# Kernel tuning notes

Measured on AMD Instinct MI355X. Metric: run time of the kernel, lower is better.

Reference implementation:

```python
import jax, jax.numpy as jnp
import numpy as np

B, S, H, FMAX, MAXSENT, NHEADS, FFN, SEP = 32, 2048, 768, 32, 64, 12, 3072, 102


def setup_inputs() -> dict:
    key = jax.random.key(0)
    ks = jax.random.split(key, 16)
    sc = 0.02
    ids = jax.random.randint(ks[0], (B, S), 1000, 30000)
    pos = jnp.arange(S)
    # SEP token every 32 positions -> 63 variable-span 'sentences' per row
    ids = jnp.where((pos[None, :] % 32 == 0) & (pos[None, :] > 0), SEP, ids)
    n = lambda k, shp: sc * jax.random.normal(k, shp, jnp.float32)
    return {
        "hidden1": jax.random.normal(ks[1], (B, S, H), jnp.float32),
        "fact_cls": jax.random.normal(ks[2], (B, FMAX, H), jnp.float32),
        "Wp": n(ks[3], (H, H)), "bp": jnp.zeros((H,), jnp.float32), "vp": n(ks[4], (H, 1)),
        "Wq": n(ks[5], (H, H)), "bq": jnp.zeros((H,), jnp.float32),
        "Wk": n(ks[6], (H, H)), "bk": jnp.zeros((H,), jnp.float32),
        "Wv": n(ks[7], (H, H)), "bv": jnp.zeros((H,), jnp.float32),
        "Wo": n(ks[8], (H, H)), "bo": jnp.zeros((H,), jnp.float32),
        "ln1g": jnp.ones((H,), jnp.float32), "ln1b": jnp.zeros((H,), jnp.float32),
        "Wf1": n(ks[9], (H, FFN)), "bf1": jnp.zeros((FFN,), jnp.float32),
        "Wf2": n(ks[10], (FFN, H)), "bf2": jnp.zeros((H,), jnp.float32),
        "ln2g": jnp.ones((H,), jnp.float32), "ln2b": jnp.zeros((H,), jnp.float32),
        "input_ids": ids,
        "facts_count": jax.random.randint(ks[11], (B,), 0, FMAX),
        "max_sent": MAXSENT,
        "sep_id": SEP,
    }


def _ln(x, g, b):
    mu = jnp.mean(x, axis=-1, keepdims=True)
    var = jnp.mean((x - mu) ** 2, axis=-1, keepdims=True)
    return (x - mu) * jax.lax.rsqrt(var + 1e-12) * g + b


def _forward(hidden1, fact_cls, Wp, bp, vp, Wq, bq, Wk, bk, Wv, bv, Wo, bo,
             ln1g, ln1b, Wf1, bf1, Wf2, bf2, ln2g, ln2b,
             input_ids, facts_count, max_sent, sep_id):
    B_, S_ = input_ids.shape
    H_ = hidden1.shape[-1]
    # ---- ragged sentence spans: tokens strictly between SEPs, starting at pos 1 ----
    is_sep = input_ids == sep_id                      # [B,S]
    n_sent = jnp.sum(is_sep, axis=-1)                 # [B]
    seg = jnp.cumsum(is_sep, axis=1) - is_sep         # exclusive cumsum: sentence id per token
    pos = jnp.arange(S_)
    valid = (pos[None, :] >= 1) & (~is_sep) & (seg < n_sent[:, None])
    nseg = B_ * max_sent
    seg_id = jnp.where(valid, jnp.arange(B_)[:, None] * max_sent + seg, nseg).reshape(-1)
    # ---- attention pooling per sentence (segment softmax) ----
    scores = jnp.squeeze(jnp.tanh(hidden1 @ Wp + bp) @ vp, -1).reshape(-1)  # [B*S]
    vflat = valid.reshape(-1)
    m = jax.ops.segment_max(scores, seg_id, num_segments=nseg + 1)
    e = jnp.where(vflat, jnp.exp(scores - m[seg_id]), 0.0)
    z = jax.ops.segment_sum(e, seg_id, num_segments=nseg + 1)
    z = jnp.where(z > 0, z, 1.0)
    w = e / z[seg_id]
    sent = jax.ops.segment_sum(w[:, None] * hidden1.reshape(-1, H_), seg_id,
                               num_segments=nseg + 1)[:nseg].reshape(B_, max_sent, H_)
    # zero-sentence rows fall back to CLS embedding in slot 0
    sent = sent.at[:, 0].set(jnp.where((n_sent == 0)[:, None], hidden1[:, 0], sent[:, 0]))
    n_eff = jnp.maximum(n_sent, 1)
    # ---- pack sentences then facts into dense zero-padded buffer ----
    FMAX_ = fact_cls.shape[1]
    L = max_sent + FMAX_
    bidx = jnp.arange(B_)[:, None]
    buf = jnp.zeros((B_, L + 1, H_), hidden1.dtype)  # extra trash column L
    spos = jnp.where(jnp.arange(max_sent)[None, :] < n_eff[:, None],
                     jnp.arange(max_sent)[None, :], L)
    buf = buf.at[bidx, spos].set(sent)
    fpos = jnp.where(jnp.arange(FMAX_)[None, :] < facts_count[:, None],
                     n_eff[:, None] + jnp.arange(FMAX_)[None, :], L)
    buf = buf.at[bidx, fpos].set(fact_cls)
    x = buf[:, :L]
    amask = (jnp.arange(L)[None, :] < (n_eff + facts_count)[:, None]).astype(x.dtype)
    # ---- tf2 encoder layer (BERT post-LN) on packed sequence ----
    nh = NHEADS
    dh = H_ // nh
    q = (x @ Wq + bq).reshape(B_, L, nh, dh)
    k = (x @ Wk + bk).reshape(B_, L, nh, dh)
    v = (x @ Wv + bv).reshape(B_, L, nh, dh)
    att = jnp.einsum('blhd,bmhd->bhlm', q, k) / np.sqrt(dh).astype(x.dtype)
    att = att + (1.0 - amask)[:, None, None, :] * jnp.asarray(-1e9, x.dtype)
    att = jax.nn.softmax(att, axis=-1)
    ctx = jnp.einsum('bhlm,bmhd->blhd', att, v).reshape(B_, L, H_)
    x = _ln(x + ctx @ Wo + bo, ln1g, ln1b)
    h = jax.nn.gelu(x @ Wf1 + bf1, approximate=False) @ Wf2 + bf2
    x = _ln(x + h, ln2g, ln2b)
    return x[:, 0, :]


def reference(hidden1, fact_cls, Wp, bp, vp, Wq, bq, Wk, bk, Wv, bv, Wo, bo,
              ln1g, ln1b, Wf1, bf1, Wf2, bf2, ln2g, ln2b,
              input_ids, facts_count, max_sent, sep_id):
    return _forward(hidden1, fact_cls, Wp, bp, vp, Wq, bq, Wk, bk, Wv, bv, Wo, bo,
                    ln1g, ln1b, Wf1, bf1, Wf2, bf2, ln2g, ln2b,
                    input_ids, facts_count, max_sent, sep_id)
```

## Files before the change

### kernel.cpp

```cpp
#include <hip/hip_runtime.h>
#include <math.h>

#define Bz   32
#define Sz   2048
#define Hz   768
#define FMAXz 32
#define MSz  64
#define NHz  12
#define DHz  64
#define Lz   96
#define FFNz 3072
#define NTOK (Bz*Sz)

typedef short bf16x8 __attribute__((ext_vector_type(8)));
typedef float f32x4 __attribute__((ext_vector_type(4)));

__device__ __forceinline__ unsigned short f2bf(float f) {
  unsigned u = __float_as_uint(f);
  unsigned r = (u + 0x7fffu + ((u >> 16) & 1u)) >> 16;
  return (unsigned short)r;
}

__device__ __forceinline__ float fast_tanh(float x) {
  float e = __expf(2.0f * x);
  return 1.0f - 2.0f / (e + 1.0f);
}

__device__ __forceinline__ void gload16(const void* gp, void* lp) {
  __builtin_amdgcn_global_load_lds(
      (const __attribute__((address_space(1))) unsigned int*)(unsigned long long)(uintptr_t)gp,
      (__attribute__((address_space(3))) unsigned int*)(unsigned int)(uintptr_t)lp,
      16, 0, 0);
}

__global__ __launch_bounds__(256) void k_seg(
    const int* __restrict__ ids, const int* __restrict__ sep_p,
    int* __restrict__ segid, int* __restrict__ seppos,
    int* __restrict__ nsent, int* __restrict__ neff)
{
  int b = blockIdx.x, tid = threadIdx.x;
  int sep = *sep_p;
  __shared__ int cnt[256];
  __shared__ int total_s;
  const int* row = &ids[b*Sz];
  int base = tid*8;
  int loc[8];
  int c = 0;
  #pragma unroll
  for (int i = 0; i < 8; i++) { loc[i] = row[base+i]; c += (loc[i]==sep) ? 1 : 0; }
  cnt[tid] = c;
  __syncthreads();
  if (tid == 0) {
    int run = 0;
    for (int t = 0; t < 256; t++) { int tmp = cnt[t]; cnt[t] = run; run += tmp; }
    total_s = run;
    nsent[b] = run;
    neff[b]  = run > 0 ? run : 1;
  }
  __syncthreads();
  int total = total_s;
  int seg = cnt[tid];
  #pragma unroll
  for (int i = 0; i < 8; i++) {
    int s = base + i;
    bool issep = (loc[i]==sep);
    if (issep && seg < MSz) seppos[b*MSz + seg] = s;
    bool valid = (s >= 1) && !issep && (seg < total);
    segid[b*Sz + s] = valid ? seg : -1;
    if (issep) seg++;
  }
}

__global__ __launch_bounds__(256) void k_cvt_bf16(
    const float* __restrict__ src, unsigned short* __restrict__ dst, int n4)
{
  int i = blockIdx.x*256 + threadIdx.x;
  if (i >= n4) return;
  float4 v = ((const float4*)src)[i];
  ushort4 o;
  o.x = f2bf(v.x); o.y = f2bf(v.y); o.z = f2bf(v.z); o.w = f2bf(v.w);
  ((ushort4*)dst)[i] = o;
}

__global__ __launch_bounds__(256) void k_tr_cvt(
    const float* __restrict__ src, unsigned short* __restrict__ dst,
    int rows, int cols)
{
  __shared__ float t[32][33];
  int c0 = blockIdx.x*32, r0 = blockIdx.y*32;
  int cx = threadIdx.x & 31, ry = threadIdx.x >> 5;
  #pragma unroll
  for (int p = 0; p < 4; p++)
    t[ry + p*8][cx] = src[(size_t)(r0 + ry + p*8)*cols + c0 + cx];
  __syncthreads();
  #pragma unroll
  for (int p = 0; p < 4; p++) {
    int i = ry + p*8;
    dst[(size_t)(c0 + i)*rows + r0 + cx] = f2bf(t[cx][i]);
  }
}

__global__ __launch_bounds__(256) void k_scores_mfma(
    const unsigned short* __restrict__ h1b, const unsigned short* __restrict__ wpT,
    const float* __restrict__ bp, const float* __restrict__ vp,
    float* __restrict__ scores)
{
  __shared__ unsigned short As[4096];
  __shared__ unsigned short Bs[4096];
  __shared__ float bps[Hz];
  __shared__ float vps[Hz];
  const int tid = threadIdx.x;
  const int wave = tid >> 6, lane = tid & 63;
  const int ml = lane & 15, kg = lane >> 4;
  const size_t tok0 = (size_t)blockIdx.x * 128;
  for (int i = tid; i < Hz; i += 256) { bps[i] = bp[i]; vps[i] = vp[i]; }
  float part[2][4] = {{0,0,0,0},{0,0,0,0}};
  for (int j0 = 0; j0 < Hz; j0 += 128) {
    f32x4 acc[2][8];
    #pragma unroll
    for (int rt = 0; rt < 2; rt++)
      #pragma unroll
      for (int ct = 0; ct < 8; ct++) acc[rt][ct] = (f32x4){0.f,0.f,0.f,0.f};
    for (int k0 = 0; k0 < Hz; k0 += 32) {
      __syncthreads();
      #pragma unroll
      for (int l = 0; l < 2; l++) {
        int slot = l*256 + tid;
        int m = slot & 127, kgs = slot >> 7;
        gload16(&h1b[(tok0 + m)*Hz + k0 + kgs*8], &As[slot*8]);
        gload16(&wpT[(size_t)(j0 + m)*Hz + k0 + kgs*8], &Bs[slot*8]);
      }
      __syncthreads();
      bf16x8 af0 = *(const bf16x8*)&As[(kg*128 + wave*32 + ml)*8];
      bf16x8 af1 = *(const bf16x8*)&As[(kg*128 + wave*32 + 16 + ml)*8];
      #pragma unroll
      for (int ct = 0; ct < 8; ct++) {
        bf16x8 bfr = *(const bf16x8*)&Bs[(kg*128 + ct*16 + ml)*8];
        acc[0][ct] = __builtin_amdgcn_mfma_f32_16x16x32_bf16(af0, bfr, acc[0][ct], 0, 0, 0);
        acc[1][ct] = __builtin_amdgcn_mfma_f32_16x16x32_bf16(af1, bfr, acc[1][ct], 0, 0, 0);
      }
    }
    #pragma unroll
    for (int ct = 0; ct < 8; ct++) {
      int col = j0 + ct*16 + ml;
      float bpv = bps[col], vpv = vps[col];
      #pragma unroll
      for (int rt = 0; rt < 2; rt++)
        #pragma unroll
        for (int i = 0; i < 4; i++)
          part[rt][i] += fast_tanh(acc[rt][ct][i] + bpv) * vpv;
    }
  }
  #pragma unroll
  for (int rt = 0; rt < 2; rt++)
    #pragma unroll
    for (int i = 0; i < 4; i++) {
      float v = part[rt][i];
      v += __shfl_xor(v, 1); v += __shfl_xor(v, 2);
      v += __shfl_xor(v, 4); v += __shfl_xor(v, 8);
      if (ml == 0) scores[tok0 + wave*32 + rt*16 + kg*4 + i] = v;
    }
}

__device__ inline unsigned fenc(float f){ unsigned u = __float_as_uint(f); return (u & 0x80000000u) ? ~u : (u | 0x80000000u); }
__device__ inline float fdec(unsigned u){ return (u & 0x80000000u) ? __uint_as_float(u & 0x7fffffffu) : __uint_as_float(~u); }

__global__ __launch_bounds__(256) void k_softmax_seg(
    const float* __restrict__ scores, const int* __restrict__ segid,
    float* __restrict__ w)
{
  int b = blockIdx.x, tid = threadIdx.x;
  __shared__ unsigned menc[MSz];
  __shared__ float msh[MSz];
  __shared__ float zsh[MSz];
  if (tid < MSz) { menc[tid] = 0u; zsh[tid] = 0.f; }
  __syncthreads();
  for (int s = tid; s < Sz; s += 256) {
    int g = segid[b*Sz + s];
    if (g >= 0 && g < MSz) atomicMax(&menc[g], fenc(scores[b*Sz+s]));
  }
  __syncthreads();
  if (tid < MSz) msh[tid] = fdec(menc[tid]);
  __syncthreads();
  for (int s = tid; s < Sz; s += 256) {
    int g = segid[b*Sz + s];
    float e = 0.f;
    if (g >= 0 && g < MSz) { e = expf(scores[b*Sz+s] - msh[g]); atomicAdd(&zsh[g], e); }
    w[b*Sz + s] = e;
  }
  __syncthreads();
  if (tid < MSz) zsh[tid] = (zsh[tid] > 0.f) ? 1.0f/zsh[tid] : 1.0f;
  __syncthreads();
  for (int s = tid; s < Sz; s += 256) {
    int g = segid[b*Sz + s];
    if (g >= 0 && g < MSz) w[b*Sz + s] *= zsh[g];
  }
}

__global__ __launch_bounds__(256) void k_sent(
    const float* __restrict__ h1, const float* __restrict__ w,
    const int* __restrict__ seppos, const int* __restrict__ nsent,
    const int* __restrict__ neff, float* __restrict__ x)
{
  int s = blockIdx.x, b = blockIdx.y, tid = threadIdx.x;
  int ne = neff[b], ns = nsent[b];
  if (s >= ne) return;
  float* xr = &x[((size_t)b*Lz + s)*Hz];
  if (ns == 0) {
    const float* hr = &h1[(size_t)b*Sz*Hz];
    xr[tid] = hr[tid]; xr[tid+256] = hr[tid+256]; xr[tid+512] = hr[tid+512];
    return;
  }
  int start = (s == 0) ? 1 : seppos[b*MSz + s - 1] + 1;
  int end = seppos[b*MSz + s];
  float a0=0.f, a1=0.f, a2=0.f;
  for (int t = start; t < end; t++) {
    float wv = w[b*Sz + t];
    const float* hr = &h1[((size_t)b*Sz + t)*Hz];
    a0 += wv*hr[tid]; a1 += wv*hr[tid+256]; a2 += wv*hr[tid+512];
  }
  xr[tid]=a0; xr[tid+256]=a1; xr[tid+512]=a2;
}

__global__ __launch_bounds__(256) void k_facts(
    const float* __restrict__ fc, const int* __restrict__ fcnt,
    const int* __restrict__ neff, float* __restrict__ x)
{
  int f = blockIdx.x, b = blockIdx.y, tid = threadIdx.x;
  if (f >= fcnt[b]) return;
  int pos = neff[b] + f;
  if (pos >= Lz) return;
  float* xr = &x[((size_t)b*Lz + pos)*Hz];
  const float* fr = &fc[((size_t)b*FMAXz + f)*Hz];
  xr[tid] = fr[tid]; xr[tid+256] = fr[tid+256]; xr[tid+512] = fr[tid+512];
}

__global__ __launch_bounds__(256) void k_packb(
    const float* __restrict__ bk, const float* __restrict__ bv, float* __restrict__ bcat)
{
  int i = blockIdx.x*256 + threadIdx.x;
  if (i < Hz) bcat[i] = bk[i];
  else if (i < 2*Hz) bcat[i] = bv[i - Hz];
}

__global__ __launch_bounds__(256) void k_kv_mfma(
    const unsigned short* __restrict__ xb, const unsigned short* __restrict__ wkvT,
    const float* __restrict__ bcat, float* __restrict__ kv)
{
  __shared__ unsigned short As[4096];
  __shared__ unsigned short Bs[4096];
  const int tid = threadIdx.x;
  const int wave = tid >> 6, lane = tid & 63;
  const int ml = lane & 15, kg = lane >> 4;
  const int j0 = blockIdx.x * 128;
  const size_t m0 = (size_t)blockIdx.y * 128;
  f32x4 acc[2][8];
  #pragma unroll
  for (int rt = 0; rt < 2; rt++)
    #pragma unroll
    for (int ct = 0; ct < 8; ct++) acc[rt][ct] = (f32x4){0.f,0.f,0.f,0.f};
  for (int k0 = 0; k0 < Hz; k0 += 32) {
    __syncthreads();
    #pragma unroll
    for (int l = 0; l < 2; l++) {
      int slot = l*256 + tid;
      int m = slot & 127, kgs = slot >> 7;
      gload16(&xb[(m0 + m)*Hz + k0 + kgs*8], &As[slot*8]);
      gload16(&wkvT[(size_t)(j0 + m)*Hz + k0 + kgs*8], &Bs[slot*8]);
    }
    __syncthreads();
    bf16x8 af0 = *(const bf16x8*)&As[(kg*128 + wave*32 + ml)*8];
    bf16x8 af1 = *(const bf16x8*)&As[(kg*128 + wave*32 + 16 + ml)*8];
    #pragma unroll
    for (int ct = 0; ct < 8; ct++) {
      bf16x8 bfr = *(const bf16x8*)&Bs[(kg*128 + ct*16 + ml)*8];
      acc[0][ct] = __builtin_amdgcn_mfma_f32_16x16x32_bf16(af0, bfr, acc[0][ct], 0, 0, 0);
      acc[1][ct] = __builtin_amdgcn_mfma_f32_16x16x32_bf16(af1, bfr, acc[1][ct], 0, 0, 0);
    }
  }
  #pragma unroll
  for (int ct = 0; ct < 8; ct++) {
    int col = j0 + ct*16 + ml;
    float bb = bcat[col];
    #pragma unroll
    for (int rt = 0; rt < 2; rt++)
      #pragma unroll
      for (int i = 0; i < 4; i++) {
        size_t row = m0 + wave*32 + rt*16 + kg*4 + i;
        kv[row*1536 + col] = acc[rt][ct][i] + bb;
      }
  }
}

__global__ __launch_bounds__(256) void k_gemv32(
    const float* __restrict__ A, int astr,
    const float* __restrict__ W,
    const float* __restrict__ bias,
    const float* __restrict__ resid, int rstride,
    float* __restrict__ C, int K, int N, int act)
{
  __shared__ float As2[32*128];
  __shared__ float red[4][16][32];
  const int tid = threadIdx.x;
  const int c = tid & 15, ks = tid >> 4;
  const int j = blockIdx.x*16 + c;
  float acc[32];
  #pragma unroll
  for (int b = 0; b < 32; b++) acc[b] = 0.f;
  for (int k0 = 0; k0 < K; k0 += 128) {
    __syncthreads();
    #pragma unroll
    for (int p = 0; p < 4; p++) {
      int e = (p*256 + tid)*4;
      int b = e >> 7, kk = e & 127;
      *(float4*)&As2[b*128+kk] = *(const float4*)&A[(size_t)b*astr + k0 + kk];
    }
    __syncthreads();
    #pragma unroll
    for (int q = 0; q < 8; q++) {
      int kk = ks*8 + q;
      float wv = W[(size_t)(k0+kk)*N + j];
      #pragma unroll
      for (int b = 0; b < 32; b++) acc[b] += As2[b*128+kk]*wv;
    }
  }
  #pragma unroll
  for (int b = 0; b < 32; b++) {
    float v = acc[b];
    v += __shfl_xor(v, 16);
    v += __shfl_xor(v, 32);
    acc[b] = v;
  }
  int wave = tid >> 6, lane = tid & 63;
  if (lane < 16) {
    #pragma unroll
    for (int b = 0; b < 32; b++) red[wave][c][b] = acc[b];
  }
  __syncthreads();
  int c2 = tid & 15, b0 = tid >> 4;
  int j2 = blockIdx.x*16 + c2;
  #pragma unroll
  for (int h = 0; h < 2; h++) {
    int b = b0 + h*16;
    float v = red[0][c2][b] + red[1][c2][b] + red[2][c2][b] + red[3][c2][b];
    v += bias[j2];
    if (resid) v += resid[(size_t)b*rstride + j2];
    if (act == 1) v = 0.5f*v*(1.0f + erff(v*0.70710678118654752f));
    C[(size_t)b*N + j2] = v;
  }
}

__global__ __launch_bounds__(128) void k_attn(
    const float* __restrict__ q0, const float* __restrict__ kv,
    const int* __restrict__ neff, const int* __restrict__ fcnt,
    float* __restrict__ ctx0)
{
  int h = blockIdx.x, b = blockIdx.y, tid = threadIdx.x;
  __shared__ float att[Lz];
  __shared__ float qsh[DHz];
  __shared__ float inv_s;
  if (tid < DHz) qsh[tid] = q0[b*Hz + h*DHz + tid];
  __syncthreads();
  int lv = neff[b] + fcnt[b];
  if (tid < Lz) {
    const float* kr = &kv[((size_t)b*Lz + tid)*1536 + h*DHz];
    float s = 0.f;
    #pragma unroll
    for (int d = 0; d < DHz; d++) s += qsh[d]*kr[d];
    s *= 0.125f;
    if (tid >= lv) s -= 1e9f;
    att[tid] = s;
  }
  __syncthreads();
  if (tid == 0) {
    float m = att[0];
    for (int i = 1; i < Lz; i++) m = fmaxf(m, att[i]);
    float z = 0.f;
    for (int i = 0; i < Lz; i++) { float e = expf(att[i] - m); att[i] = e; z += e; }
    inv_s = 1.f/z;
  }
  __syncthreads();
  float inv = inv_s;
  if (tid < DHz) {
    float cvv = 0.f;
    for (int m2 = 0; m2 < Lz; m2++)
      cvv += att[m2] * kv[((size_t)b*Lz + m2)*1536 + Hz + h*DHz + tid];
    ctx0[b*Hz + h*DHz + tid] = cvv*inv;
  }
}

__device__ inline float block_sum_256(float v, float* red)
{
  int tid = threadIdx.x;
  red[tid] = v; __syncthreads();
  for (int off = 128; off > 0; off >>= 1) {
    if (tid < off) red[tid] += red[tid + off];
    __syncthreads();
  }
  float r = red[0];
  __syncthreads();
  return r;
}

__global__ __launch_bounds__(256) void k_ln32(
    const float* __restrict__ in, const float* __restrict__ g,
    const float* __restrict__ bt, float* __restrict__ out)
{
  int b = blockIdx.x, tid = threadIdx.x;
  __shared__ float red[256];
  float a0 = in[b*Hz+tid], a1 = in[b*Hz+tid+256], a2 = in[b*Hz+tid+512];
  float mu = block_sum_256(a0+a1+a2, red) * (1.0f/Hz);
  float d0=a0-mu, d1=a1-mu, d2=a2-mu;
  float var = block_sum_256(d0*d0+d1*d1+d2*d2, red) * (1.0f/Hz);
  float rs = rsqrtf(var + 1e-12f);
  out[b*Hz+tid]     = d0*rs*g[tid]     + bt[tid];
  out[b*Hz+tid+256] = d1*rs*g[tid+256] + bt[tid+256];
  out[b*Hz+tid+512] = d2*rs*g[tid+512] + bt[tid+512];
}

extern "C" void kernel_launch(void* const* d_in, const int* in_sizes, int n_in,
                              void* d_out, int out_size, void* d_ws, size_t ws_size,
                              hipStream_t stream)
{
  (void)in_sizes; (void)n_in; (void)out_size; (void)ws_size;
  const float* hidden1  = (const float*)d_in[0];
  const float* fact_cls = (const float*)d_in[1];
  const float* Wp   = (const float*)d_in[2];
  const float* bp   = (const float*)d_in[3];
  const float* vp   = (const float*)d_in[4];
  const float* Wq   = (const float*)d_in[5];
  const float* bq   = (const float*)d_in[6];
  const float* Wk   = (const float*)d_in[7];
  const float* bk   = (const float*)d_in[8];
  const float* Wv   = (const float*)d_in[9];
  const float* bv   = (const float*)d_in[10];
  const float* Wo   = (const float*)d_in[11];
  const float* bo   = (const float*)d_in[12];
  const float* ln1g = (const float*)d_in[13];
  const float* ln1b = (const float*)d_in[14];
  const float* Wf1  = (const float*)d_in[15];
  const float* bf1  = (const float*)d_in[16];
  const float* Wf2  = (const float*)d_in[17];
  const float* bf2  = (const float*)d_in[18];
  const float* ln2g = (const float*)d_in[19];
  const float* ln2b = (const float*)d_in[20];
  const int* input_ids   = (const int*)d_in[21];
  const int* facts_count = (const int*)d_in[22];
  const int* sep_id      = (const int*)d_in[24];

  char* ws = (char*)d_ws;
  size_t off = 0;
  auto alloc = [&](size_t bytes) -> void* {
    void* p = ws + off; off += (bytes + 255) & ~(size_t)255; return p;
  };
  unsigned short* h1b  = (unsigned short*)alloc(sizeof(short)*(size_t)NTOK*Hz);
  unsigned short* wpT  = (unsigned short*)alloc(sizeof(short)*(size_t)Hz*Hz);
  unsigned short* wkvT = (unsigned short*)alloc(sizeof(short)*(size_t)Hz*1536);
  unsigned short* xb   = (unsigned short*)alloc(sizeof(short)*(size_t)Bz*Lz*Hz);
  float* x      = (float*)alloc(sizeof(float)*(size_t)Bz*Lz*Hz);
  float* kv     = (float*)alloc(sizeof(float)*(size_t)Bz*Lz*1536);
  float* bcat   = (float*)alloc(sizeof(float)*1536);
  float* scores = (float*)alloc(sizeof(float)*NTOK);
  float* w      = (float*)alloc(sizeof(float)*NTOK);
  int*   segid  = (int*)alloc(sizeof(int)*NTOK);
  int*   seppos = (int*)alloc(sizeof(int)*Bz*MSz);
  int*   nsent  = (int*)alloc(sizeof(int)*Bz);
  int*   neff   = (int*)alloc(sizeof(int)*Bz);
  float* q0     = (float*)alloc(sizeof(float)*Bz*Hz);
  float* ctx0   = (float*)alloc(sizeof(float)*Bz*Hz);
  float* tmp0   = (float*)alloc(sizeof(float)*Bz*Hz);
  float* y0     = (float*)alloc(sizeof(float)*Bz*Hz);
  float* tmp1   = (float*)alloc(sizeof(float)*Bz*Hz);
  float* ffnmid = (float*)alloc(sizeof(float)*Bz*FFNz);

  k_cvt_bf16<<<(NTOK*Hz/4 + 255)/256, 256, 0, stream>>>(hidden1, h1b, NTOK*Hz/4);
  k_tr_cvt<<<dim3(Hz/32, Hz/32), 256, 0, stream>>>(Wp, wpT, Hz, Hz);
  k_seg<<<Bz, 256, 0, stream>>>(input_ids, sep_id, segid, seppos, nsent, neff);

  k_scores_mfma<<<NTOK/128, 256, 0, stream>>>(h1b, wpT, bp, vp, scores);
  k_softmax_seg<<<Bz, 256, 0, stream>>>(scores, segid, w);

  hipMemsetAsync(x, 0, sizeof(float)*(size_t)Bz*Lz*Hz, stream);
  k_sent<<<dim3(MSz, Bz), 256, 0, stream>>>(hidden1, w, seppos, nsent, neff, x);
  k_facts<<<dim3(FMAXz, Bz), 256, 0, stream>>>(fact_cls, facts_count, neff, x);
  k_cvt_bf16<<<(Bz*Lz*Hz/4 + 255)/256, 256, 0, stream>>>(x, xb, Bz*Lz*Hz/4);

  k_tr_cvt<<<dim3(Hz/32, Hz/32), 256, 0, stream>>>(Wk, wkvT, Hz, Hz);
  k_tr_cvt<<<dim3(Hz/32, Hz/32), 256, 0, stream>>>(Wv, wkvT + (size_t)Hz*Hz, Hz, Hz);
  k_packb<<<6, 256, 0, stream>>>(bk, bv, bcat);
  k_kv_mfma<<<dim3(12, Bz*Lz/128), 256, 0, stream>>>(xb, wkvT, bcat, kv);

  k_gemv32<<<Hz/16, 256, 0, stream>>>(x, Lz*Hz, Wq, bq, nullptr, 0, q0, Hz, Hz, 0);
  k_attn<<<dim3(NHz, Bz), 128, 0, stream>>>(q0, kv, neff, facts_count, ctx0);
  k_gemv32<<<Hz/16, 256, 0, stream>>>(ctx0, Hz, Wo, bo, x, Lz*Hz, tmp0, Hz, Hz, 0);
  k_ln32<<<Bz, 256, 0, stream>>>(tmp0, ln1g, ln1b, y0);

  k_gemv32<<<FFNz/16, 256, 0, stream>>>(y0, Hz, Wf1, bf1, nullptr, 0, ffnmid, Hz, FFNz, 1);
  k_gemv32<<<Hz/16, 256, 0, stream>>>(ffnmid, FFNz, Wf2, bf2, y0, Hz, tmp1, FFNz, Hz, 0);
  k_ln32<<<Bz, 256, 0, stream>>>(tmp1, ln2g, ln2b, (float*)d_out);
}
```

Baseline: 721.2 us.

## Split scores GEMM over column tiles and split-K the small GEMV chain

The scores kernel now gets a 2D grid, so each block handles one 128-column slice of Wp and adds its tanh·v partial into scores with atomics, after a memset. This raises the block count six-fold, but the same activation tile is reloaded for every column slice. The four batch-32 GEMVs are rewritten as split-K partial kernels with 64-column tiles. Bias, residual and GELU are folded into the consumers (attention, LayerNorm and the next GEMV's input load), which adds parallelism for these tiny GEMVs at the cost of extra partial-sum traffic and repeated erf work.

```diff
diff --git a/kernel.cpp b/kernel.cpp
--- a/kernel.cpp
+++ b/kernel.cpp
@@ -107,49 +107,47 @@
 {
   __shared__ unsigned short As[4096];
   __shared__ unsigned short Bs[4096];
-  __shared__ float bps[Hz];
-  __shared__ float vps[Hz];
+  __shared__ float bps[128], vps[128];
   const int tid = threadIdx.x;
   const int wave = tid >> 6, lane = tid & 63;
   const int ml = lane & 15, kg = lane >> 4;
-  const size_t tok0 = (size_t)blockIdx.x * 128;
-  for (int i = tid; i < Hz; i += 256) { bps[i] = bp[i]; vps[i] = vp[i]; }
+  const int j0 = blockIdx.x * 128;
+  const size_t tok0 = (size_t)blockIdx.y * 128;
+  if (tid < 128) { bps[tid] = bp[j0+tid]; vps[tid] = vp[j0+tid]; }
+  f32x4 acc[2][8];
+  #pragma unroll
+  for (int rt = 0; rt < 2; rt++)
+    #pragma unroll
+    for (int ct = 0; ct < 8; ct++) acc[rt][ct] = (f32x4){0.f,0.f,0.f,0.f};
+  for (int k0 = 0; k0 < Hz; k0 += 32) {
+    __syncthreads();
+    #pragma unroll
+    for (int l = 0; l < 2; l++) {
+      int slot = l*256 + tid;
+      int m = slot & 127, kgs = slot >> 7;
+      gload16(&h1b[(tok0 + m)*Hz + k0 + kgs*8], &As[slot*8]);
+      gload16(&wpT[(size_t)(j0 + m)*Hz + k0 + kgs*8], &Bs[slot*8]);
+    }
+    __syncthreads();
+    bf16x8 af0 = *(const bf16x8*)&As[(kg*128 + wave*32 + ml)*8];
+    bf16x8 af1 = *(const bf16x8*)&As[(kg*128 + wave*32 + 16 + ml)*8];
+    #pragma unroll
+    for (int ct = 0; ct < 8; ct++) {
+      bf16x8 bfr = *(const bf16x8*)&Bs[(kg*128 + ct*16 + ml)*8];
+      acc[0][ct] = __builtin_amdgcn_mfma_f32_16x16x32_bf16(af0, bfr, acc[0][ct], 0, 0, 0);
+      acc[1][ct] = __builtin_amdgcn_mfma_f32_16x16x32_bf16(af1, bfr, acc[1][ct], 0, 0, 0);
+    }
+  }
   float part[2][4] = {{0,0,0,0},{0,0,0,0}};
-  for (int j0 = 0; j0 < Hz; j0 += 128) {
-    f32x4 acc[2][8];
+  #pragma unroll
+  for (int ct = 0; ct < 8; ct++) {
+    int cl = ct*16 + ml;
+    float bpv = bps[cl], vpv = vps[cl];
     #pragma unroll
     for (int rt = 0; rt < 2; rt++)
       #pragma unroll
-      for (int ct = 0; ct < 8; ct++) acc[rt][ct] = (f32x4){0.f,0.f,0.f,0.f};
-    for (int k0 = 0; k0 < Hz; k0 += 32) {
-      __syncthreads();
-      #pragma unroll
-      for (int l = 0; l < 2; l++) {
-        int slot = l*256 + tid;
-        int m = slot & 127, kgs = slot >> 7;
-        gload16(&h1b[(tok0 + m)*Hz + k0 + kgs*8], &As[slot*8]);
-        gload16(&wpT[(size_t)(j0 + m)*Hz + k0 + kgs*8], &Bs[slot*8]);
-      }
-      __syncthreads();
-      bf16x8 af0 = *(const bf16x8*)&As[(kg*128 + wave*32 + ml)*8];
-      bf16x8 af1 = *(const bf16x8*)&As[(kg*128 + wave*32 + 16 + ml)*8];
-      #pragma unroll
-      for (int ct = 0; ct < 8; ct++) {
-        bf16x8 bfr = *(const bf16x8*)&Bs[(kg*128 + ct*16 + ml)*8];
-        acc[0][ct] = __builtin_amdgcn_mfma_f32_16x16x32_bf16(af0, bfr, acc[0][ct], 0, 0, 0);
-        acc[1][ct] = __builtin_amdgcn_mfma_f32_16x16x32_bf16(af1, bfr, acc[1][ct], 0, 0, 0);
-      }
-    }
-    #pragma unroll
-    for (int ct = 0; ct < 8; ct++) {
-      int col = j0 + ct*16 + ml;
-      float bpv = bps[col], vpv = vps[col];
-      #pragma unroll
-      for (int rt = 0; rt < 2; rt++)
-        #pragma unroll
-        for (int i = 0; i < 4; i++)
-          part[rt][i] += fast_tanh(acc[rt][ct][i] + bpv) * vpv;
-    }
+      for (int i = 0; i < 4; i++)
+        part[rt][i] += fast_tanh(acc[rt][ct][i] + bpv) * vpv;
   }
   #pragma unroll
   for (int rt = 0; rt < 2; rt++)
@@ -158,7 +156,7 @@
       float v = part[rt][i];
       v += __shfl_xor(v, 1); v += __shfl_xor(v, 2);
       v += __shfl_xor(v, 4); v += __shfl_xor(v, 8);
-      if (ml == 0) scores[tok0 + wave*32 + rt*16 + kg*4 + i] = v;
+      if (ml == 0) atomicAdd(&scores[tok0 + wave*32 + rt*16 + kg*4 + i], v);
     }
 }
 
@@ -292,66 +290,63 @@
   }
 }
 
-__global__ __launch_bounds__(256) void k_gemv32(
-    const float* __restrict__ A, int astr,
-    const float* __restrict__ W,
-    const float* __restrict__ bias,
-    const float* __restrict__ resid, int rstride,
-    float* __restrict__ C, int K, int N, int act)
-{
-  __shared__ float As2[32*128];
-  __shared__ float red[4][16][32];
+__global__ __launch_bounds__(256) void k_gemv_part(
+    const float* __restrict__ A, int astr, int aparts, const float* __restrict__ abias,
+    int agelu, const float* __restrict__ W, float* __restrict__ part, int N)
+{
+  __shared__ float As2[32*196];
+  __shared__ float red[4][32][64];
   const int tid = threadIdx.x;
-  const int c = tid & 15, ks = tid >> 4;
-  const int j = blockIdx.x*16 + c;
+  const int k0 = blockIdx.y * 192;
+  {
+    int b = tid >> 3, t8 = tid & 7;
+    #pragma unroll
+    for (int i = 0; i < 24; i++) {
+      int kk = t8*24 + i;
+      float v;
+      if (aparts == 0) {
+        v = A[(size_t)b*astr + k0 + kk];
+      } else {
+        v = abias[k0 + kk];
+        for (int p = 0; p < aparts; p++) v += A[((size_t)p*32 + b)*astr + k0 + kk];
+        if (agelu) v = 0.5f*v*(1.0f + erff(v*0.70710678118654752f));
+      }
+      As2[b*196 + kk] = v;
+    }
+  }
+  __syncthreads();
+  const int jc = tid & 63, w = tid >> 6;
+  const int j = blockIdx.x*64 + jc;
   float acc[32];
   #pragma unroll
   for (int b = 0; b < 32; b++) acc[b] = 0.f;
-  for (int k0 = 0; k0 < K; k0 += 128) {
-    __syncthreads();
-    #pragma unroll
-    for (int p = 0; p < 4; p++) {
-      int e = (p*256 + tid)*4;
-      int b = e >> 7, kk = e & 127;
-      *(float4*)&As2[b*128+kk] = *(const float4*)&A[(size_t)b*astr + k0 + kk];
-    }
-    __syncthreads();
-    #pragma unroll
-    for (int q = 0; q < 8; q++) {
-      int kk = ks*8 + q;
-      float wv = W[(size_t)(k0+kk)*N + j];
-      #pragma unroll
-      for (int b = 0; b < 32; b++) acc[b] += As2[b*128+kk]*wv;
-    }
-  }
-  #pragma unroll
-  for (int b = 0; b < 32; b++) {
-    float v = acc[b];
-    v += __shfl_xor(v, 16);
-    v += __shfl_xor(v, 32);
-    acc[b] = v;
-  }
-  int wave = tid >> 6, lane = tid & 63;
-  if (lane < 16) {
-    #pragma unroll
-    for (int b = 0; b < 32; b++) red[wave][c][b] = acc[b];
-  }
-  __syncthreads();
-  int c2 = tid & 15, b0 = tid >> 4;
-  int j2 = blockIdx.x*16 + c2;
-  #pragma unroll
-  for (int h = 0; h < 2; h++) {
-    int b = b0 + h*16;
-    float v = red[0][c2][b] + red[1][c2][b] + red[2][c2][b] + red[3][c2][b];
-    v += bias[j2];
-    if (resid) v += resid[(size_t)b*rstride + j2];
-    if (act == 1) v = 0.5f*v*(1.0f + erff(v*0.70710678118654752f));
-    C[(size_t)b*N + j2] = v;
+  for (int kq = 0; kq < 12; kq++) {
+    int kk = w*48 + kq*4;
+    float w0 = W[(size_t)(k0+kk  )*N + j];
+    float w1 = W[(size_t)(k0+kk+1)*N + j];
+    float w2 = W[(size_t)(k0+kk+2)*N + j];
+    float w3 = W[(size_t)(k0+kk+3)*N + j];
+    #pragma unroll
+    for (int b = 0; b < 32; b++) {
+      float4 a = *(const float4*)&As2[b*196 + kk];
+      acc[b] += a.x*w0 + a.y*w1 + a.z*w2 + a.w*w3;
+    }
+  }
+  #pragma unroll
+  for (int b = 0; b < 32; b++) red[w][b][jc] = acc[b];
+  __syncthreads();
+  #pragma unroll
+  for (int r = 0; r < 8; r++) {
+    int o = r*256 + tid;
+    int b = o >> 6, jc2 = o & 63;
+    float s = red[0][b][jc2] + red[1][b][jc2] + red[2][b][jc2] + red[3][b][jc2];
+    part[((size_t)blockIdx.y*32 + b)*N + blockIdx.x*64 + jc2] = s;
   }
 }
 
 __global__ __launch_bounds__(128) void k_attn(
-    const float* __restrict__ q0, const float* __restrict__ kv,
+    const float* __restrict__ qpart, const float* __restrict__ bq,
+    const float* __restrict__ kv,
     const int* __restrict__ neff, const int* __restrict__ fcnt,
     float* __restrict__ ctx0)
 {
@@ -359,7 +354,13 @@
   __shared__ float att[Lz];
   __shared__ float qsh[DHz];
   __shared__ float inv_s;
-  if (tid < DHz) qsh[tid] = q0[b*Hz + h*DHz + tid];
+  if (tid < DHz) {
+    int col = h*DHz + tid;
+    float qv = bq[col];
+    #pragma unroll
+    for (int p = 0; p < 4; p++) qv += qpart[((size_t)p*32 + b)*Hz + col];
+    qsh[tid] = qv;
+  }
   __syncthreads();
   int lv = neff[b] + fcnt[b];
   if (tid < Lz) {
@@ -402,13 +403,22 @@
   return r;
 }
 
-__global__ __launch_bounds__(256) void k_ln32(
-    const float* __restrict__ in, const float* __restrict__ g,
-    const float* __restrict__ bt, float* __restrict__ out)
+__global__ __launch_bounds__(256) void k_ln32_fold(
+    const float* __restrict__ part, int P,
+    const float* __restrict__ bias,
+    const float* __restrict__ resid, int rstr,
+    const float* __restrict__ g, const float* __restrict__ bt,
+    float* __restrict__ out)
 {
   int b = blockIdx.x, tid = threadIdx.x;
   __shared__ float red[256];
-  float a0 = in[b*Hz+tid], a1 = in[b*Hz+tid+256], a2 = in[b*Hz+tid+512];
+  float a0 = bias[tid]     + resid[(size_t)b*rstr + tid];
+  float a1 = bias[tid+256] + resid[(size_t)b*rstr + tid+256];
+  float a2 = bias[tid+512] + resid[(size_t)b*rstr + tid+512];
+  for (int p = 0; p < P; p++) {
+    const float* pr = &part[((size_t)p*32 + b)*Hz];
+    a0 += pr[tid]; a1 += pr[tid+256]; a2 += pr[tid+512];
+  }
   float mu = block_sum_256(a0+a1+a2, red) * (1.0f/Hz);
   float d0=a0-mu, d1=a1-mu, d2=a2-mu;
   float var = block_sum_256(d0*d0+d1*d1+d2*d2, red) * (1.0f/Hz);
@@ -466,18 +476,19 @@
   int*   seppos = (int*)alloc(sizeof(int)*Bz*MSz);
   int*   nsent  = (int*)alloc(sizeof(int)*Bz);
   int*   neff   = (int*)alloc(sizeof(int)*Bz);
-  float* q0     = (float*)alloc(sizeof(float)*Bz*Hz);
+  float* qpart  = (float*)alloc(sizeof(float)*4*Bz*Hz);
   float* ctx0   = (float*)alloc(sizeof(float)*Bz*Hz);
-  float* tmp0   = (float*)alloc(sizeof(float)*Bz*Hz);
+  float* wopart = (float*)alloc(sizeof(float)*4*Bz*Hz);
   float* y0     = (float*)alloc(sizeof(float)*Bz*Hz);
-  float* tmp1   = (float*)alloc(sizeof(float)*Bz*Hz);
-  float* ffnmid = (float*)alloc(sizeof(float)*Bz*FFNz);
+  float* fpart  = (float*)alloc(sizeof(float)*4*Bz*FFNz);
+  float* f2part = (float*)alloc(sizeof(float)*16*Bz*Hz);
 
   k_cvt_bf16<<<(NTOK*Hz/4 + 255)/256, 256, 0, stream>>>(hidden1, h1b, NTOK*Hz/4);
   k_tr_cvt<<<dim3(Hz/32, Hz/32), 256, 0, stream>>>(Wp, wpT, Hz, Hz);
   k_seg<<<Bz, 256, 0, stream>>>(input_ids, sep_id, segid, seppos, nsent, neff);
 
-  k_scores_mfma<<<NTOK/128, 256, 0, stream>>>(h1b, wpT, bp, vp, scores);
+  hipMemsetAsync(scores, 0, sizeof(float)*NTOK, stream);
+  k_scores_mfma<<<dim3(6, NTOK/128), 256, 0, stream>>>(h1b, wpT, bp, vp, scores);
   k_softmax_seg<<<Bz, 256, 0, stream>>>(scores, segid, w);
 
   hipMemsetAsync(x, 0, sizeof(float)*(size_t)Bz*Lz*Hz, stream);
@@ -490,12 +501,12 @@
   k_packb<<<6, 256, 0, stream>>>(bk, bv, bcat);
   k_kv_mfma<<<dim3(12, Bz*Lz/128), 256, 0, stream>>>(xb, wkvT, bcat, kv);
 
-  k_gemv32<<<Hz/16, 256, 0, stream>>>(x, Lz*Hz, Wq, bq, nullptr, 0, q0, Hz, Hz, 0);
-  k_attn<<<dim3(NHz, Bz), 128, 0, stream>>>(q0, kv, neff, facts_count, ctx0);
-  k_gemv32<<<Hz/16, 256, 0, stream>>>(ctx0, Hz, Wo, bo, x, Lz*Hz, tmp0, Hz, Hz, 0);
-  k_ln32<<<Bz, 256, 0, stream>>>(tmp0, ln1g, ln1b, y0);
-
-  k_gemv32<<<FFNz/16, 256, 0, stream>>>(y0, Hz, Wf1, bf1, nullptr, 0, ffnmid, Hz, FFNz, 1);
-  k_gemv32<<<Hz/16, 256, 0, stream>>>(ffnmid, FFNz, Wf2, bf2, y0, Hz, tmp1, FFNz, Hz, 0);
-  k_ln32<<<Bz, 256, 0, stream>>>(tmp1, ln2g, ln2b, (float*)d_out);
-}
+  k_gemv_part<<<dim3(Hz/64, 4), 256, 0, stream>>>(x, Lz*Hz, 0, nullptr, 0, Wq, qpart, Hz);
+  k_attn<<<dim3(NHz, Bz), 128, 0, stream>>>(qpart, bq, kv, neff, facts_count, ctx0);
+  k_gemv_part<<<dim3(Hz/64, 4), 256, 0, stream>>>(ctx0, Hz, 0, nullptr, 0, Wo, wopart, Hz);
+  k_ln32_fold<<<Bz, 256, 0, stream>>>(wopart, 4, bo, x, Lz*Hz, ln1g, ln1b, y0);
+
+  k_gemv_part<<<dim3(FFNz/64, 4), 256, 0, stream>>>(y0, Hz, 0, nullptr, 0, Wf1, fpart, FFNz);
+  k_gemv_part<<<dim3(Hz/64, 16), 256, 0, stream>>>(fpart, FFNz, 4, bf1, 1, Wf2, f2part, Hz);
+  k_ln32_fold<<<Bz, 256, 0, stream>>>(f2part, 16, bf2, y0, Hz, ln2g, ln2b, (float*)d_out);
+}
```

New measurement: 718.3 us. Within noise of the previous version (-0.4%).
